# Performance work log

Measured on AMD Instinct MI355X. Metric: run time of the kernel, lower is better.

The kernel has to match this reference:

```python
import jax, jax.numpy as jnp
import numpy as np


def ste_sign(w):
    # straight-through binarization: forward sign(w), backward identity
    return w + jax.lax.stop_gradient(jnp.sign(w) - w)


def spike(x):
    # Heaviside spike with straight-through estimator
    return x + jax.lax.stop_gradient((x > 0).astype(x.dtype) - x)


def quantized_conv1d(x, w, b, stride, padding):
    # XNOR-Net style 1-bit weights: sign(w) * per-out-channel mean(|w|)
    alpha = jnp.mean(jnp.abs(w), axis=(1, 2), keepdims=True)  # (O,1,1)
    wq = ste_sign(w) * alpha
    y = jax.lax.conv_general_dilated(
        x, wq, window_strides=(stride,), padding=[(padding, padding)],
        dimension_numbers=('NCH', 'OIH', 'NCH'))
    return y + b[None, :, None]


def batchnorm(x, gamma, beta, eps=1e-5):
    # training-mode BN over (batch, length) per channel
    mu = jnp.mean(x, axis=(0, 2), keepdims=True)
    var = jnp.var(x, axis=(0, 2), keepdims=True)
    return (x - mu) * jax.lax.rsqrt(var + eps) * gamma[None, :, None] + beta[None, :, None]


def window_attn(sq, sk, sv, w):
    # spiking attention restricted to non-overlapping windows of size w
    B, L, C = sq.shape
    pad = (-L) % w
    p = lambda a: jnp.pad(a, ((0, 0), (0, pad), (0, 0)))  # zero-pad -> zero spikes
    q = p(sq).reshape(B, -1, w, C)
    k = p(sk).reshape(B, -1, w, C)
    v = p(sv).reshape(B, -1, w, C)
    attn = jnp.einsum('bnwc,bnuc->bnwu', q, k)           # (B, nW, w, w)
    out = jnp.einsum('bnwu,bnuc->bnwc', attn, v) / w
    return out.reshape(B, -1, C)[:, :L]


def global_attn(sq, K, V, g):
    # pool K,V down to g global tokens, then linear spiking attention
    B, L, C = K.shape
    chunk = -(-L // g)
    pad = chunk * g - L
    p = lambda a: jnp.pad(a, ((0, 0), (0, pad), (0, 0)))
    kp = p(K).reshape(B, g, chunk, C).mean(axis=2)       # (B, g, C)
    vp = p(V).reshape(B, g, chunk, C).mean(axis=2)
    skg, svg = spike(kp), spike(vp)
    kv = jnp.einsum('bgc,bgd->bcd', skg, svg)            # (B, C, C)
    return jnp.einsum('blc,bcd->bld', sq, kv) / g


def mssa(x, wq, wk, wv, wo, local_w=64, regional_w=256, global_pool=16):
    # x: (B, C, L) -> token-major (B, L, C)
    h = jnp.swapaxes(x, 1, 2)
    Q, K, V = h @ wq, h @ wk, h @ wv
    sq, sk, sv = spike(Q), spike(K), spike(V)
    out = (window_attn(sq, sk, sv, local_w)
           + window_attn(sq, sk, sv, regional_w)
           + global_attn(sq, K, V, global_pool)) / 3.0
    y = h + out @ wo  # residual
    return jnp.swapaxes(y, 1, 2)


def setup_inputs() -> dict:
    key = jax.random.key(0)
    ks = jax.random.split(key, 8)
    B, Cin, L, Cout = 32, 256, 5000, 128
    return {
        'x': jax.random.normal(ks[0], (B, Cin, L), jnp.float32),
        'conv_w': jax.random.normal(ks[1], (Cout, Cin, 9), jnp.float32) * 0.05,
        'conv_b': jnp.zeros((Cout,), jnp.float32),
        'gamma': jnp.ones((Cout,), jnp.float32),
        'beta': jnp.zeros((Cout,), jnp.float32),
        'wq': jax.random.normal(ks[2], (Cout, Cout), jnp.float32) * 0.09,
        'wk': jax.random.normal(ks[3], (Cout, Cout), jnp.float32) * 0.09,
        'wv': jax.random.normal(ks[4], (Cout, Cout), jnp.float32) * 0.09,
        'wo': jax.random.normal(ks[5], (Cout, Cout), jnp.float32) * 0.09,
    }


def reference(x, conv_w, conv_b, gamma, beta, wq, wk, wv, wo):
    y = quantized_conv1d(x, conv_w, conv_b, stride=2, padding=4)  # (B,128,2500)
    y = jax.nn.elu(batchnorm(y, gamma, beta))
    return mssa(y, wq, wk, wv, wo)                                # (B,128,2500)
```

## Files before the change

### kernel.cpp

```cpp
#include <hip/hip_runtime.h>

typedef __attribute__((ext_vector_type(8))) short bf16x8;
typedef __attribute__((ext_vector_type(4))) float f32x4;
typedef __attribute__((ext_vector_type(16))) float f32x16;
typedef __attribute__((ext_vector_type(4))) unsigned int u32x4;
typedef unsigned short u16;
typedef unsigned int u32;

#define DI __device__ __forceinline__

constexpr int B_ = 32, CI = 256, LX = 5000, CO = 128, LO = 2500, KW = 9, LP = 2560;

DI float b2f(u16 u) { u32 x = ((u32)u) << 16; return __builtin_bit_cast(float, x); }
DI u16 f2b(float f) {
  u32 x = __builtin_bit_cast(u32, f);
  u32 r = (x + 0x7fffu + ((x >> 16) & 1u)) >> 16;
  return (u16)r;
}
DI float elu(float v) { return v > 0.f ? v : expm1f(v); }

__global__ __launch_bounds__(256) void k_prep_wq(const float* __restrict__ w, u16* __restrict__ wfmt,
                                                 float* __restrict__ alphaf) {
  int o = blockIdx.x;
  const float* wrow = w + o * CI * KW;
  float s = 0.f;
  for (int idx = threadIdx.x; idx < CI * KW; idx += 256) s += fabsf(wrow[idx]);
  __shared__ float red[256];
  red[threadIdx.x] = s;
  __syncthreads();
  for (int st = 128; st > 0; st >>= 1) {
    if (threadIdx.x < st) red[threadIdx.x] += red[threadIdx.x + st];
    __syncthreads();
  }
  if (threadIdx.x == 0) alphaf[o] = red[0] / (float)(CI * KW);
  for (int idx = threadIdx.x; idx < CI * KW; idx += 256) {
    int i = idx / KW, k = idx - i * KW;
    float v = wrow[idx];
    float sg = v > 0.f ? 1.f : (v < 0.f ? -1.f : 0.f);
    wfmt[(((k * 16) + (i >> 4)) * 128 + o) * 16 + (i & 15)] = f2b(sg);
  }
}

__global__ __launch_bounds__(256) void k_prep_wT(const float* __restrict__ wq, const float* __restrict__ wk,
                                                 const float* __restrict__ wv, const float* __restrict__ wo,
                                                 u16* __restrict__ wThi, u16* __restrict__ wTlo,
                                                 u16* __restrict__ wT3) {
  const float* src[4] = {wq, wk, wv, wo};
  int mat = blockIdx.x;
  const float* m = src[mat];
  u16* dh = wThi + mat * CO * CO;
  u16* dl = wTlo + mat * CO * CO;
  for (int idx = threadIdx.x; idx < CO * CO; idx += 256) {
    int nn = idx >> 7, kkn = idx & 127;
    float v = m[kkn * CO + nn];
    u16 hi = f2b(v);
    u16 lo = f2b(v - b2f(hi));
    dh[idx] = hi;
    dl[idx] = lo;
    if (mat < 3) {
      int nt = nn >> 4, n = nn & 15, ks = kkn >> 5, gj = kkn & 31;
      size_t base = (size_t)((mat * 4 + ks) * 8 + nt) * 1024 + n * 32 + gj;
      wT3[base] = hi;
      wT3[base + 512] = lo;
    }
  }
}

__global__ __launch_bounds__(512) void k_conv(const float* __restrict__ x, const u16* __restrict__ wfmt,
                                              const float* __restrict__ bias, const float* __restrict__ alphaf,
                                              float* __restrict__ y1) {
  const int ltile = blockIdx.x, b = blockIdx.y;
  const int l0 = ltile * 64;
  const int lin0 = 2 * l0 - 4;
  alignas(16) __shared__ u16 xsh[136 * 136];
  alignas(16) __shared__ u16 xsl[136 * 136];
  const int tid = threadIdx.x;
  const int wave = tid >> 6, lane = tid & 63;
  const int col = lane & 31, g = lane >> 5;
  const int o0 = (wave & 3) * 32;
  const int lw = (wave >> 2) * 32;
  f32x16 acch = {};
  f32x16 accl = {};
  for (int cpass = 0; cpass < 2; ++cpass) {
    const int c0 = cpass * 128;
    if (cpass) __syncthreads();
#pragma unroll
    for (int it = 0; it < 9; ++it) {
      int idx = tid + it * 512;
      if (idx < 4352) {
        int i = idx / 34, q = idx - i * 34;
        int lin = lin0 + q * 4;
        const float* xr = x + ((size_t)(b * CI + c0 + i)) * LX;
        float4 v4 = float4{0.f, 0.f, 0.f, 0.f};
        if (lin >= 0 && lin + 4 <= LX) v4 = *reinterpret_cast<const float4*>(xr + lin);
        const float* vp = reinterpret_cast<const float*>(&v4);
#pragma unroll
        for (int e = 0; e < 4; ++e) {
          int p = q * 4 + e;
          float v = vp[e];
          u16 hi = f2b(v);
          int colx = ((((i >> 3) ^ ((p >> 1) & 15)) & 15) << 3) | (i & 7);
          xsh[p * 136 + colx] = hi;
          xsl[p * 136 + colx] = f2b(v - b2f(hi));
        }
      }
    }
    __syncthreads();
    for (int kk = 0; kk < KW; ++kk) {
      bf16x8 af[8];
#pragma unroll
      for (int icg = 0; icg < 8; ++icg) {
        int chunk = kk * 16 + cpass * 8 + icg;
        af[icg] = *reinterpret_cast<const bf16x8*>(wfmt + ((size_t)chunk * 128 + o0 + col) * 16 + g * 8);
      }
      const int p = 2 * (lw + col) + kk;
      const int prow = p * 136;
      const int s = (p >> 1) & 15;
#pragma unroll
      for (int icg = 0; icg < 8; ++icg) {
        int blkoff = (((icg * 2 + g) ^ s) << 3);
        bf16x8 bh = *reinterpret_cast<const bf16x8*>(&xsh[prow + blkoff]);
        bf16x8 bl = *reinterpret_cast<const bf16x8*>(&xsl[prow + blkoff]);
        acch = __builtin_amdgcn_mfma_f32_32x32x16_bf16(af[icg], bh, acch, 0, 0, 0);
        accl = __builtin_amdgcn_mfma_f32_32x32x16_bf16(af[icg], bl, accl, 0, 0, 0);
      }
    }
  }
  const int l = l0 + lw + col;
  if (l < LO) {
#pragma unroll
    for (int r = 0; r < 16; ++r) {
      int o = o0 + (r & 3) + 8 * (r >> 2) + 4 * g;
      y1[(b * CO + o) * LO + l] = alphaf[o] * (acch[r] + accl[r]) + bias[o];
    }
  }
}

__global__ __launch_bounds__(256) void k_stats(const float* __restrict__ y1, float* __restrict__ ps,
                                               float* __restrict__ ps2) {
  int o = blockIdx.x, b = blockIdx.y;
  const float4* row = reinterpret_cast<const float4*>(y1 + (size_t)(b * CO + o) * LO);
  float s = 0.f, s2 = 0.f;
  for (int i = threadIdx.x; i < 625; i += 256) {
    float4 v = row[i];
    s += v.x + v.y + v.z + v.w;
    s2 += v.x * v.x + v.y * v.y + v.z * v.z + v.w * v.w;
  }
  __shared__ float r1[256], r2[256];
  r1[threadIdx.x] = s;
  r2[threadIdx.x] = s2;
  __syncthreads();
  for (int st = 128; st > 0; st >>= 1) {
    if (threadIdx.x < st) {
      r1[threadIdx.x] += r1[threadIdx.x + st];
      r2[threadIdx.x] += r2[threadIdx.x + st];
    }
    __syncthreads();
  }
  if (threadIdx.x == 0) {
    ps[b * CO + o] = r1[0];
    ps2[b * CO + o] = r2[0];
  }
}

__global__ void k_bnparams(const float* __restrict__ ps, const float* __restrict__ ps2,
                           const float* __restrict__ gamma, const float* __restrict__ beta,
                           float* __restrict__ bnsc, float* __restrict__ bnsh) {
  int o = threadIdx.x;
  float s = 0.f, s2 = 0.f;
  for (int b = 0; b < B_; ++b) {
    s += ps[b * CO + o];
    s2 += ps2[b * CO + o];
  }
  const float inv_n = 1.f / (float)(B_ * LO);
  float mu = s * inv_n;
  float var = s2 * inv_n - mu * mu;
  float sc = gamma[o] * rsqrtf(var + 1e-5f);
  bnsc[o] = sc;
  bnsh[o] = beta[o] - mu * sc;
}

__global__ __launch_bounds__(256) void k_qkv(const float* __restrict__ y1, const float* __restrict__ bnsc,
                                             const float* __restrict__ bnsh, const u16* __restrict__ wT3,
                                             u16* __restrict__ sq, u16* __restrict__ sk, u16* __restrict__ sv) {
  int tile = blockIdx.x, b = blockIdx.y;
  int tid = threadIdx.x, wave = tid >> 6, lane = tid & 63, n = lane & 15, g = lane >> 4;
  const int t0 = tile * 64;
  alignas(16) __shared__ u16 hshi[64 * 136];
  alignas(16) __shared__ u16 hslo[64 * 136];
  {
    int t = tid & 63;
    int l = t0 + t;
    if (l > LO - 1) l = LO - 1;
    for (int c = (tid >> 6); c < CO; c += 4) {
      float raw = y1[((size_t)b * CO + c) * LO + l];
      float e = elu(raw * bnsc[c] + bnsh[c]);
      u16 hi = f2b(e);
      hshi[t * 136 + c] = hi;
      hslo[t * 136 + c] = f2b(e - b2f(hi));
    }
  }
  __syncthreads();
  const u16* ah = &hshi[(wave * 16 + n) * 136];
  const u16* al = &hslo[(wave * 16 + n) * 136];
  u16* outs[3] = {sq, sk, sv};
  for (int mat = 0; mat < 3; ++mat) {
    f32x4 acc[8] = {};
#pragma unroll
    for (int ks = 0; ks < 4; ++ks) {
      bf16x8 ahi = *reinterpret_cast<const bf16x8*>(ah + ks * 32 + g * 8);
      bf16x8 alo = *reinterpret_cast<const bf16x8*>(al + ks * 32 + g * 8);
      const u16* wbase = wT3 + (size_t)((mat * 4 + ks) * 8) * 1024 + n * 32 + g * 8;
#pragma unroll
      for (int nt = 0; nt < 8; ++nt) {
        bf16x8 bhi = *reinterpret_cast<const bf16x8*>(wbase + nt * 1024);
        bf16x8 blo = *reinterpret_cast<const bf16x8*>(wbase + nt * 1024 + 512);
        acc[nt] = __builtin_amdgcn_mfma_f32_16x16x32_bf16(ahi, bhi, acc[nt], 0, 0, 0);
        acc[nt] = __builtin_amdgcn_mfma_f32_16x16x32_bf16(ahi, blo, acc[nt], 0, 0, 0);
        acc[nt] = __builtin_amdgcn_mfma_f32_16x16x32_bf16(alo, bhi, acc[nt], 0, 0, 0);
        acc[nt] = __builtin_amdgcn_mfma_f32_16x16x32_bf16(alo, blo, acc[nt], 0, 0, 0);
      }
    }
    u16* so = outs[mat];
#pragma unroll
    for (int nt = 0; nt < 8; ++nt) {
#pragma unroll
      for (int r = 0; r < 4; ++r) {
        int tok = t0 + wave * 16 + g * 4 + r;
        int c = nt * 16 + n;
        bool valid = tok < LO;
        float v = valid ? acc[nt][r] : 0.f;
        so[((size_t)b * LP + tok) * CO + c] = f2b(v > 0.f ? 1.f : 0.f);
      }
    }
  }
}

__global__ __launch_bounds__(64) void k_poolh(const float* __restrict__ y1, const float* __restrict__ bnsc,
                                              const float* __restrict__ bnsh, float* __restrict__ hsum) {
  int c = blockIdx.x, b = blockIdx.y, lane = threadIdx.x;
  const float* row = y1 + ((size_t)b * CO + c) * LO;
  const float sc = bnsc[c], sh = bnsh[c];
  __shared__ float bins[16][64];
#pragma unroll
  for (int ch = 0; ch < 16; ++ch) bins[ch][lane] = 0.f;
  for (int j = lane; j < LO; j += 64) {
    float e = elu(row[j] * sc + sh);
    bins[j / 157][lane] += e;
  }
#pragma unroll
  for (int ch = 0; ch < 16; ++ch) {
    float v = bins[ch][lane];
    for (int off = 32; off > 0; off >>= 1) v += __shfl_down(v, off);
    if (lane == 0) hsum[(b * 16 + ch) * CO + c] = v;
  }
}

__global__ __launch_bounds__(256) void k_kv2(const float* __restrict__ hsum, const float* __restrict__ wk,
                                             const float* __restrict__ wv, u16* __restrict__ kvT) {
  int b = blockIdx.x;
  __shared__ float hs[16 * 128], sks[16 * 128], svs[16 * 128];
  for (int i = threadIdx.x; i < 2048; i += 256) hs[i] = hsum[b * 2048 + i];
  __syncthreads();
  for (int idx = threadIdx.x; idx < 2048; idx += 256) {
    int gg = idx >> 7, c = idx & 127;
    float ak = 0.f, av = 0.f;
    for (int k = 0; k < 128; ++k) {
      float hv = hs[gg * 128 + k];
      ak += hv * wk[k * CO + c];
      av += hv * wv[k * CO + c];
    }
    sks[idx] = ak > 0.f ? 1.f : 0.f;
    svs[idx] = av > 0.f ? 1.f : 0.f;
  }
  __syncthreads();
  for (int idx = threadIdx.x; idx < CO * CO; idx += 256) {
    int d = idx >> 7, c = idx & 127;
    float s = 0.f;
#pragma unroll
    for (int gg = 0; gg < 16; ++gg) s += sks[gg * 128 + c] * svs[gg * 128 + d];
    kvT[b * CO * CO + idx] = f2b(s * (1.f / 48.f));
  }
}

__global__ __launch_bounds__(512) void k_attn(const u16* __restrict__ sq, const u16* __restrict__ sk,
                                              const u16* __restrict__ sv, const u16* __restrict__ kvT,
                                              const u16* __restrict__ woT, const float* __restrict__ y1,
                                              const float* __restrict__ bnsc, const float* __restrict__ bnsh,
                                              float* __restrict__ out) {
  const int win = blockIdx.x, b = blockIdx.y, qt = blockIdx.z;
  const int T0 = win * 256;
  alignas(16) __shared__ char smem[69632];
  u16* svT = reinterpret_cast<u16*>(smem);
  const int tid = threadIdx.x, wave = tid >> 6, lane = tid & 63, n = lane & 15, g = lane >> 4;
  for (int idx = tid; idx < 256 * 128; idx += 512) {
    int u = idx >> 7, c = idx & 127;
    svT[c * 264 + u] = sv[((size_t)b * LP + T0 + u) * CO + c];
  }
  __syncthreads();
  {
    const int qbase = wave * 32 + qt * 16;
    bf16x8 bq[4];
    const u16* qrow = sq + ((size_t)b * LP + T0 + qbase + n) * CO;
#pragma unroll
    for (int ks = 0; ks < 4; ++ks) bq[ks] = *reinterpret_cast<const bf16x8*>(qrow + ks * 32 + g * 8);
    f32x4 pacc[16];
#pragma unroll
    for (int ut = 0; ut < 16; ++ut) pacc[ut] = f32x4{0.f, 0.f, 0.f, 0.f};
    for (int ut = 0; ut < 16; ++ut) {
      const u16* krow = sk + ((size_t)b * LP + T0 + ut * 16 + n) * CO;
#pragma unroll
      for (int ks = 0; ks < 4; ++ks) {
        bf16x8 af = *reinterpret_cast<const bf16x8*>(krow + ks * 32 + g * 8);
        pacc[ut] = __builtin_amdgcn_mfma_f32_16x16x32_bf16(af, bq[ks], pacc[ut], 0, 0, 0);
      }
    }
    const int qblk = (qbase + n) >> 6;
    u32 packed[16][2];
#pragma unroll
    for (int ut = 0; ut < 16; ++ut) {
      u16 pk[4];
#pragma unroll
      for (int r = 0; r < 4; ++r) {
        int uloc = ut * 16 + g * 4 + r;
        float wgt = (1.f / 768.f) + (((uloc >> 6) == qblk) ? (1.f / 192.f) : 0.f);
        pk[r] = f2b(pacc[ut][r] * wgt);
      }
      packed[ut][0] = (u32)pk[0] | ((u32)pk[1] << 16);
      packed[ut][1] = (u32)pk[2] | ((u32)pk[3] << 16);
    }
    const int sl0 = n + 16 * ((g & 1) * 2);
    const int sl1 = sl0 + 16;
    const bool ghi = ((g >> 1) & 1) != 0;
    f32x4 acco[8] = {};
#pragma unroll
    for (int us = 0; us < 8; ++us) {
      u32 a0e = (u32)__shfl((int)packed[us * 2][0], sl0, 64);
      u32 a0o = (u32)__shfl((int)packed[us * 2 + 1][0], sl0, 64);
      u32 a1e = (u32)__shfl((int)packed[us * 2][1], sl0, 64);
      u32 a1o = (u32)__shfl((int)packed[us * 2 + 1][1], sl0, 64);
      u32 a2e = (u32)__shfl((int)packed[us * 2][0], sl1, 64);
      u32 a2o = (u32)__shfl((int)packed[us * 2 + 1][0], sl1, 64);
      u32 a3e = (u32)__shfl((int)packed[us * 2][1], sl1, 64);
      u32 a3o = (u32)__shfl((int)packed[us * 2 + 1][1], sl1, 64);
      u32x4 paw = {ghi ? a0o : a0e, ghi ? a1o : a1e, ghi ? a2o : a2e, ghi ? a3o : a3e};
      bf16x8 pa = __builtin_bit_cast(bf16x8, paw);
#pragma unroll
      for (int ct = 0; ct < 8; ++ct) {
        bf16x8 bv = *reinterpret_cast<const bf16x8*>(&svT[(ct * 16 + n) * 264 + us * 32 + g * 8]);
        acco[ct] = __builtin_amdgcn_mfma_f32_16x16x32_bf16(pa, bv, acco[ct], 0, 0, 0);
      }
    }
#pragma unroll
    for (int ks = 0; ks < 4; ++ks) {
#pragma unroll
      for (int ct = 0; ct < 8; ++ct) {
        bf16x8 bkv = *reinterpret_cast<const bf16x8*>(kvT + ((size_t)b * CO + ct * 16 + n) * CO + ks * 32 + g * 8);
        acco[ct] = __builtin_amdgcn_mfma_f32_16x16x32_bf16(bq[ks], bkv, acco[ct], 0, 0, 0);
      }
    }
    __syncthreads();
    u16* pw2 = reinterpret_cast<u16*>(smem) + wave * (16 * 136);
    float* sF = reinterpret_cast<float*>(smem + 34816) + wave * (64 * 17);
#pragma unroll
    for (int ct = 0; ct < 8; ++ct) {
#pragma unroll
      for (int r = 0; r < 4; ++r) {
        pw2[(g * 4 + r) * 136 + ct * 16 + n] = f2b(acco[ct][r]);
      }
    }
    for (int half = 0; half < 2; ++half) {
#pragma unroll
      for (int ot2 = 0; ot2 < 4; ++ot2) {
        int ot = half * 4 + ot2;
        f32x4 facc = {};
#pragma unroll
        for (int ks = 0; ks < 4; ++ks) {
          bf16x8 af = *reinterpret_cast<const bf16x8*>(&pw2[n * 136 + ks * 32 + g * 8]);
          bf16x8 bw = *reinterpret_cast<const bf16x8*>(woT + (ot * 16 + n) * CO + ks * 32 + g * 8);
          facc = __builtin_amdgcn_mfma_f32_16x16x32_bf16(af, bw, facc, 0, 0, 0);
        }
#pragma unroll
        for (int r = 0; r < 4; ++r) sF[(ot2 * 16 + n) * 17 + g * 4 + r] = facc[r];
      }
#pragma unroll
      for (int oo = 0; oo < 16; ++oo) {
        int olocal = oo * 4 + (lane >> 4);
        int o = half * 64 + olocal;
        int l = T0 + qbase + (lane & 15);
        float v = sF[olocal * 17 + (lane & 15)];
        if (l < LO) {
          size_t idx = ((size_t)b * CO + o) * LO + l;
          out[idx] = elu(y1[idx] * bnsc[o] + bnsh[o]) + v;
        }
      }
    }
  }
}

extern "C" void kernel_launch(void* const* d_in, const int* in_sizes, int n_in, void* d_out, int out_size,
                              void* d_ws, size_t ws_size, hipStream_t stream) {
  const float* x = (const float*)d_in[0];
  const float* conv_w = (const float*)d_in[1];
  const float* conv_b = (const float*)d_in[2];
  const float* gamma = (const float*)d_in[3];
  const float* beta = (const float*)d_in[4];
  const float* wq = (const float*)d_in[5];
  const float* wk = (const float*)d_in[6];
  const float* wv = (const float*)d_in[7];
  const float* wo = (const float*)d_in[8];
  (void)in_sizes; (void)n_in; (void)out_size; (void)ws_size;

  char* ws = (char*)d_ws;
  size_t off = 0;
  auto alloc = [&](size_t bytes) -> void* {
    void* p = ws + off;
    off += (bytes + 511) & ~(size_t)511;
    return p;
  };
  float* ps = (float*)alloc((size_t)B_ * CO * 4);
  float* ps2 = (float*)alloc((size_t)B_ * CO * 4);
  float* bnsc = (float*)alloc(CO * 4);
  float* bnsh = (float*)alloc(CO * 4);
  float* alphaf = (float*)alloc(CO * 4);
  float* hsum = (float*)alloc((size_t)B_ * 16 * CO * 4);
  u16* kvT = (u16*)alloc((size_t)B_ * CO * CO * 2);
  u16* wfmt = (u16*)alloc((size_t)CO * KW * CI * 2);
  u16* wThi = (u16*)alloc((size_t)4 * CO * CO * 2);
  u16* wTlo = (u16*)alloc((size_t)4 * CO * CO * 2);
  u16* wT3 = (u16*)alloc((size_t)3 * 4 * 8 * 1024 * 2);
  float* y1 = (float*)alloc((size_t)B_ * CO * LO * 4);
  u16* sqb = (u16*)alloc((size_t)B_ * LP * CO * 2);
  u16* skb = (u16*)alloc((size_t)B_ * LP * CO * 2);
  u16* svb = (u16*)alloc((size_t)B_ * LP * CO * 2);

  hipLaunchKernelGGL(k_prep_wq, dim3(CO), dim3(256), 0, stream, conv_w, wfmt, alphaf);
  hipLaunchKernelGGL(k_prep_wT, dim3(4), dim3(256), 0, stream, wq, wk, wv, wo, wThi, wTlo, wT3);
  hipLaunchKernelGGL(k_conv, dim3(40, B_), dim3(512), 0, stream, x, wfmt, conv_b, alphaf, y1);
  hipLaunchKernelGGL(k_stats, dim3(CO, B_), dim3(256), 0, stream, y1, ps, ps2);
  hipLaunchKernelGGL(k_bnparams, dim3(1), dim3(CO), 0, stream, ps, ps2, gamma, beta, bnsc, bnsh);
  hipLaunchKernelGGL(k_qkv, dim3(40, B_), dim3(256), 0, stream, y1, bnsc, bnsh, wT3, sqb, skb, svb);
  hipLaunchKernelGGL(k_poolh, dim3(CO, B_), dim3(64), 0, stream, y1, bnsc, bnsh, hsum);
  hipLaunchKernelGGL(k_kv2, dim3(B_), dim3(256), 0, stream, hsum, wk, wv, kvT);
  hipLaunchKernelGGL(k_attn, dim3(10, B_, 2), dim3(512), 0, stream, sqb, skb, svb, kvT, wThi + 3 * CO * CO, y1,
                     bnsc, bnsh, (float*)d_out);
}
```

Measured before the change: 499.2 us.

## Store Q/K spikes and global KV as int8 and use i8 MFMA for scores

Spike tensors Q and K and the global KV matrix now use int8 storage instead of bf16. The QK^T score and the global-attention Q·KV products switch to i32 16x16x64 int8 MFMA. This halves the memory traffic for sq/sk/kv and cuts the MFMA count for those products. The values are exact 0/1 and small integer counts (at most 16), so int8 keeps them exact. V stays bf16 for the probability-times-V product, and the global term now seeds the output accumulator before the PV loop.

```diff
diff --git a/kernel.cpp b/kernel.cpp
--- a/kernel.cpp
+++ b/kernel.cpp
@@ -4,6 +4,7 @@
 typedef __attribute__((ext_vector_type(4))) float f32x4;
 typedef __attribute__((ext_vector_type(16))) float f32x16;
 typedef __attribute__((ext_vector_type(4))) unsigned int u32x4;
+typedef __attribute__((ext_vector_type(4))) int s32x4;
 typedef unsigned short u16;
 typedef unsigned int u32;
 
@@ -182,7 +183,8 @@
 
 __global__ __launch_bounds__(256) void k_qkv(const float* __restrict__ y1, const float* __restrict__ bnsc,
                                              const float* __restrict__ bnsh, const u16* __restrict__ wT3,
-                                             u16* __restrict__ sq, u16* __restrict__ sk, u16* __restrict__ sv) {
+                                             signed char* __restrict__ sq8, signed char* __restrict__ sk8,
+                                             u16* __restrict__ sv) {
   int tile = blockIdx.x, b = blockIdx.y;
   int tid = threadIdx.x, wave = tid >> 6, lane = tid & 63, n = lane & 15, g = lane >> 4;
   const int t0 = tile * 64;
@@ -203,7 +205,6 @@
   __syncthreads();
   const u16* ah = &hshi[(wave * 16 + n) * 136];
   const u16* al = &hslo[(wave * 16 + n) * 136];
-  u16* outs[3] = {sq, sk, sv};
   for (int mat = 0; mat < 3; ++mat) {
     f32x4 acc[8] = {};
 #pragma unroll
@@ -221,7 +222,6 @@
         acc[nt] = __builtin_amdgcn_mfma_f32_16x16x32_bf16(alo, blo, acc[nt], 0, 0, 0);
       }
     }
-    u16* so = outs[mat];
 #pragma unroll
     for (int nt = 0; nt < 8; ++nt) {
 #pragma unroll
@@ -230,7 +230,13 @@
         int c = nt * 16 + n;
         bool valid = tok < LO;
         float v = valid ? acc[nt][r] : 0.f;
-        so[((size_t)b * LP + tok) * CO + c] = f2b(v > 0.f ? 1.f : 0.f);
+        size_t oidx = ((size_t)b * LP + tok) * CO + c;
+        if (mat == 2) {
+          sv[oidx] = f2b(v > 0.f ? 1.f : 0.f);
+        } else {
+          signed char* so8 = (mat == 0) ? sq8 : sk8;
+          so8[oidx] = v > 0.f ? 1 : 0;
+        }
       }
     }
   }
@@ -257,7 +263,7 @@
 }
 
 __global__ __launch_bounds__(256) void k_kv2(const float* __restrict__ hsum, const float* __restrict__ wk,
-                                             const float* __restrict__ wv, u16* __restrict__ kvT) {
+                                             const float* __restrict__ wv, signed char* __restrict__ kv8) {
   int b = blockIdx.x;
   __shared__ float hs[16 * 128], sks[16 * 128], svs[16 * 128];
   for (int i = threadIdx.x; i < 2048; i += 256) hs[i] = hsum[b * 2048 + i];
@@ -279,12 +285,13 @@
     float s = 0.f;
 #pragma unroll
     for (int gg = 0; gg < 16; ++gg) s += sks[gg * 128 + c] * svs[gg * 128 + d];
-    kvT[b * CO * CO + idx] = f2b(s * (1.f / 48.f));
-  }
-}
-
-__global__ __launch_bounds__(512) void k_attn(const u16* __restrict__ sq, const u16* __restrict__ sk,
-                                              const u16* __restrict__ sv, const u16* __restrict__ kvT,
+    kv8[b * CO * CO + idx] = (signed char)s;
+  }
+}
+
+__global__ __launch_bounds__(512) void k_attn(const signed char* __restrict__ sq8,
+                                              const signed char* __restrict__ sk8,
+                                              const u16* __restrict__ sv, const signed char* __restrict__ kv8,
                                               const u16* __restrict__ woT, const float* __restrict__ y1,
                                               const float* __restrict__ bnsc, const float* __restrict__ bnsh,
                                               float* __restrict__ out) {
@@ -300,20 +307,19 @@
   __syncthreads();
   {
     const int qbase = wave * 32 + qt * 16;
-    bf16x8 bq[4];
-    const u16* qrow = sq + ((size_t)b * LP + T0 + qbase + n) * CO;
-#pragma unroll
-    for (int ks = 0; ks < 4; ++ks) bq[ks] = *reinterpret_cast<const bf16x8*>(qrow + ks * 32 + g * 8);
-    f32x4 pacc[16];
-#pragma unroll
-    for (int ut = 0; ut < 16; ++ut) pacc[ut] = f32x4{0.f, 0.f, 0.f, 0.f};
+    s32x4 bq8[2];
+    const signed char* qrow = sq8 + ((size_t)b * LP + T0 + qbase + n) * CO;
+    bq8[0] = *reinterpret_cast<const s32x4*>(qrow + g * 16);
+    bq8[1] = *reinterpret_cast<const s32x4*>(qrow + 64 + g * 16);
+    s32x4 pacc[16];
+#pragma unroll
+    for (int ut = 0; ut < 16; ++ut) pacc[ut] = s32x4{0, 0, 0, 0};
     for (int ut = 0; ut < 16; ++ut) {
-      const u16* krow = sk + ((size_t)b * LP + T0 + ut * 16 + n) * CO;
-#pragma unroll
-      for (int ks = 0; ks < 4; ++ks) {
-        bf16x8 af = *reinterpret_cast<const bf16x8*>(krow + ks * 32 + g * 8);
-        pacc[ut] = __builtin_amdgcn_mfma_f32_16x16x32_bf16(af, bq[ks], pacc[ut], 0, 0, 0);
-      }
+      const signed char* krow = sk8 + ((size_t)b * LP + T0 + ut * 16 + n) * CO;
+      s32x4 kf0 = *reinterpret_cast<const s32x4*>(krow + g * 16);
+      s32x4 kf1 = *reinterpret_cast<const s32x4*>(krow + 64 + g * 16);
+      pacc[ut] = __builtin_amdgcn_mfma_i32_16x16x64_i8(kf0, bq8[0], pacc[ut], 0, 0, 0);
+      pacc[ut] = __builtin_amdgcn_mfma_i32_16x16x64_i8(kf1, bq8[1], pacc[ut], 0, 0, 0);
     }
     const int qblk = (qbase + n) >> 6;
     u32 packed[16][2];
@@ -324,15 +330,26 @@
       for (int r = 0; r < 4; ++r) {
         int uloc = ut * 16 + g * 4 + r;
         float wgt = (1.f / 768.f) + (((uloc >> 6) == qblk) ? (1.f / 192.f) : 0.f);
-        pk[r] = f2b(pacc[ut][r] * wgt);
+        pk[r] = f2b((float)pacc[ut][r] * wgt);
       }
       packed[ut][0] = (u32)pk[0] | ((u32)pk[1] << 16);
       packed[ut][1] = (u32)pk[2] | ((u32)pk[3] << 16);
+    }
+    f32x4 acco[8];
+#pragma unroll
+    for (int ct = 0; ct < 8; ++ct) {
+      s32x4 ag = {0, 0, 0, 0};
+      const signed char* kvrow = kv8 + ((size_t)b * CO + ct * 16 + n) * CO;
+      s32x4 k0 = *reinterpret_cast<const s32x4*>(kvrow + g * 16);
+      s32x4 k1 = *reinterpret_cast<const s32x4*>(kvrow + 64 + g * 16);
+      ag = __builtin_amdgcn_mfma_i32_16x16x64_i8(bq8[0], k0, ag, 0, 0, 0);
+      ag = __builtin_amdgcn_mfma_i32_16x16x64_i8(bq8[1], k1, ag, 0, 0, 0);
+#pragma unroll
+      for (int r = 0; r < 4; ++r) acco[ct][r] = (float)ag[r] * (1.f / 48.f);
     }
     const int sl0 = n + 16 * ((g & 1) * 2);
     const int sl1 = sl0 + 16;
     const bool ghi = ((g >> 1) & 1) != 0;
-    f32x4 acco[8] = {};
 #pragma unroll
     for (int us = 0; us < 8; ++us) {
       u32 a0e = (u32)__shfl((int)packed[us * 2][0], sl0, 64);
@@ -349,14 +366,6 @@
       for (int ct = 0; ct < 8; ++ct) {
         bf16x8 bv = *reinterpret_cast<const bf16x8*>(&svT[(ct * 16 + n) * 264 + us * 32 + g * 8]);
         acco[ct] = __builtin_amdgcn_mfma_f32_16x16x32_bf16(pa, bv, acco[ct], 0, 0, 0);
-      }
-    }
-#pragma unroll
-    for (int ks = 0; ks < 4; ++ks) {
-#pragma unroll
-      for (int ct = 0; ct < 8; ++ct) {
-        bf16x8 bkv = *reinterpret_cast<const bf16x8*>(kvT + ((size_t)b * CO + ct * 16 + n) * CO + ks * 32 + g * 8);
-        acco[ct] = __builtin_amdgcn_mfma_f32_16x16x32_bf16(bq[ks], bkv, acco[ct], 0, 0, 0);
       }
     }
     __syncthreads();
@@ -424,14 +433,14 @@
   float* bnsh = (float*)alloc(CO * 4);
   float* alphaf = (float*)alloc(CO * 4);
   float* hsum = (float*)alloc((size_t)B_ * 16 * CO * 4);
-  u16* kvT = (u16*)alloc((size_t)B_ * CO * CO * 2);
+  signed char* kv8 = (signed char*)alloc((size_t)B_ * CO * CO);
   u16* wfmt = (u16*)alloc((size_t)CO * KW * CI * 2);
   u16* wThi = (u16*)alloc((size_t)4 * CO * CO * 2);
   u16* wTlo = (u16*)alloc((size_t)4 * CO * CO * 2);
   u16* wT3 = (u16*)alloc((size_t)3 * 4 * 8 * 1024 * 2);
   float* y1 = (float*)alloc((size_t)B_ * CO * LO * 4);
-  u16* sqb = (u16*)alloc((size_t)B_ * LP * CO * 2);
-  u16* skb = (u16*)alloc((size_t)B_ * LP * CO * 2);
+  signed char* sqb8 = (signed char*)alloc((size_t)B_ * LP * CO);
+  signed char* skb8 = (signed char*)alloc((size_t)B_ * LP * CO);
   u16* svb = (u16*)alloc((size_t)B_ * LP * CO * 2);
 
   hipLaunchKernelGGL(k_prep_wq, dim3(CO), dim3(256), 0, stream, conv_w, wfmt, alphaf);
@@ -439,9 +448,9 @@
   hipLaunchKernelGGL(k_conv, dim3(40, B_), dim3(512), 0, stream, x, wfmt, conv_b, alphaf, y1);
   hipLaunchKernelGGL(k_stats, dim3(CO, B_), dim3(256), 0, stream, y1, ps, ps2);
   hipLaunchKernelGGL(k_bnparams, dim3(1), dim3(CO), 0, stream, ps, ps2, gamma, beta, bnsc, bnsh);
-  hipLaunchKernelGGL(k_qkv, dim3(40, B_), dim3(256), 0, stream, y1, bnsc, bnsh, wT3, sqb, skb, svb);
+  hipLaunchKernelGGL(k_qkv, dim3(40, B_), dim3(256), 0, stream, y1, bnsc, bnsh, wT3, sqb8, skb8, svb);
   hipLaunchKernelGGL(k_poolh, dim3(CO, B_), dim3(64), 0, stream, y1, bnsc, bnsh, hsum);
-  hipLaunchKernelGGL(k_kv2, dim3(B_), dim3(256), 0, stream, hsum, wk, wv, kvT);
-  hipLaunchKernelGGL(k_attn, dim3(10, B_, 2), dim3(512), 0, stream, sqb, skb, svb, kvT, wThi + 3 * CO * CO, y1,
-                     bnsc, bnsh, (float*)d_out);
-}
+  hipLaunchKernelGGL(k_kv2, dim3(B_), dim3(256), 0, stream, hsum, wk, wv, kv8);
+  hipLaunchKernelGGL(k_attn, dim3(10, B_, 2), dim3(512), 0, stream, sqb8, skb8, svb, kv8, wThi + 3 * CO * CO,
+                     y1, bnsc, bnsh, (float*)d_out);
+}
```

Measured after the change: 469.2 us. 1.06x faster.
